# Performance work log

Hardware: AMD Instinct MI355X
Metric: run time of the kernel (lower is better)

Reference implementation:

```python
import jax, jax.numpy as jnp
import numpy as np

TEMPERATURE = 0.1
NEG_INF = -1e30


def setup_inputs() -> dict:
    key = jax.random.key(0)
    kf, kl = jax.random.split(key)
    N, D = 8192, 128
    features = jax.random.normal(kf, (N, D), dtype=jnp.float32)
    # labels in [-1, 80): -1 marks background rows that are filtered out
    labels = jax.random.randint(kl, (N,), -1, 80)
    return {"features": features, "labels": labels}


def reference(features, labels):
    N = labels.shape[0]
    fg = labels >= 0  # [N]

    # F.normalize(p=2, dim=1): x / max(||x||, eps)
    norm = jnp.maximum(jnp.linalg.norm(features, axis=1, keepdims=True), 1e-12)
    f = features / norm

    sim = jnp.matmul(f, f.T) / TEMPERATURE  # [N, N]

    pair_fg = fg[:, None] & fg[None, :]
    eye = jnp.eye(N, dtype=bool)
    label_eq = labels[:, None] == labels[None, :]
    pos_mask = pair_fg & label_eq & ~eye          # positives (same label, not self)
    all_mask = pair_fg & ~eye                     # pos | neg == everything but self (within fg)

    # row-wise masked max, clamped to [-20, 20] as in the original
    max_sim = jnp.max(jnp.where(all_mask, sim, NEG_INF), axis=1)
    max_sim = jnp.clip(max_sim, -20.0, 20.0)

    e = jnp.exp(sim - max_sim[:, None])           # cos-sim/temp is bounded, no overflow
    pos_sum = jnp.clip(jnp.sum(jnp.where(pos_mask, e, 0.0), axis=1), 1e-6, 1e6)
    all_sum = jnp.clip(jnp.sum(jnp.where(all_mask, e, 0.0), axis=1), 1e-6, 1e6)

    loss_i = jnp.minimum(-jnp.log(pos_sum / all_sum), 10.0)  # clamp(max=10)

    # rows contributing to the mean: fg rows with at least one positive
    valid = fg & (jnp.sum(pos_mask, axis=1) > 0)
    n_valid = jnp.sum(valid)
    mean_loss = jnp.sum(jnp.where(valid, loss_i, 0.0)) / jnp.maximum(n_valid, 1).astype(jnp.float32)

    ok = (jnp.sum(fg) >= 2) & (n_valid > 0)
    return jnp.where(ok, mean_loss, jnp.float32(0.0))
```

## Files before the change

kernel.cpp:

```cpp
#include <hip/hip_runtime.h>

#define N 8192
#define D 128
#define CHUNK 512
#define NCHUNK (N / CHUNK)
#define TILE_IT (CHUNK / 128)
#define NBIN 81
#define NBLK 512

typedef unsigned short u16;
typedef __attribute__((ext_vector_type(8))) __bf16 bf16x8;
typedef __attribute__((ext_vector_type(4))) float f32x4;

#define PREP_SCALE 3.7982889979f

__device__ __forceinline__ u16 f2bf(float x) {
  unsigned u = __float_as_uint(x);
  u += 0x7fff + ((u >> 16) & 1);
  return (u16)(u >> 16);
}
__device__ __forceinline__ float bf2f(u16 h) {
  return __uint_as_float(((unsigned)h) << 16);
}

__global__ __launch_bounds__(256) void cpe_prep(const float* __restrict__ feat,
                                                const int* __restrict__ labels,
                                                u16* __restrict__ fhi,
                                                u16* __restrict__ flo,
                                                int* __restrict__ slab,
                                                float* __restrict__ pacc,
                                                unsigned* __restrict__ ctr) {
  __shared__ int hist[4][NBIN], part[4][NBIN], lbase[NBIN], lpos[16];
  const int tid = threadIdx.x;
  const int w = tid >> 6, l = tid & 63;
  const int bid = blockIdx.x;
  if (tid < NBIN) {
#pragma unroll
    for (int cp = 0; cp < 4; ++cp) { hist[cp][tid] = 0; part[cp][tid] = 0; }
  }
  if (tid < 32) pacc[bid * 32 + tid] = 0.0f;
  if (bid == 0 && tid == 0) *ctr = 0u;
  __syncthreads();
  const int myBase = bid * 16;
  for (int j = tid; j < N; j += 256) {
    const int lab = labels[j] + 1;
    atomicAdd(&hist[w][lab], 1);
    if (j < myBase) atomicAdd(&part[w][lab], 1);
  }
  __syncthreads();
  if (tid < NBIN) {
    hist[0][tid] += hist[1][tid] + hist[2][tid] + hist[3][tid];
    part[0][tid] += part[1][tid] + part[2][tid] + part[3][tid];
  }
  __syncthreads();
  if (tid == 0) {
    int s = 0;
    for (int b = 0; b < NBIN; ++b) { lbase[b] = s; s += hist[0][b]; }
  }
  __syncthreads();
  if (tid < 16) {
    const int L = labels[myBase + tid] + 1;
    int pos = lbase[L] + part[0][L];
    for (int k = 0; k < tid; ++k) pos += (labels[myBase + k] + 1 == L) ? 1 : 0;
    lpos[tid] = pos;
    slab[pos] = L - 1;
  }
  __syncthreads();
#pragma unroll
  for (int rr = 0; rr < 4; ++rr) {
    const int k = w * 4 + rr;
    const float2 x = *(const float2*)&feat[(myBase + k) * D + l * 2];
    float s = x.x * x.x + x.y * x.y;
#pragma unroll
    for (int sh = 1; sh < 64; sh <<= 1) s += __shfl_xor(s, sh);
    const float inv = PREP_SCALE / fmaxf(sqrtf(s), 1e-12f);
    const float a = x.x * inv, b = x.y * inv;
    const u16 ah = f2bf(a), bh = f2bf(b);
    const u16 al = f2bf(a - bf2f(ah)), bl = f2bf(b - bf2f(bh));
    const int pos = lpos[k];
    *(ushort2*)&fhi[pos * D + l * 2] = make_ushort2(ah, bh);
    *(ushort2*)&flo[pos * D + l * 2] = make_ushort2(al, bl);
  }
}

__global__ __launch_bounds__(256, 2) void cpe_main(
    const u16* __restrict__ fhi, const u16* __restrict__ flo,
    const int* __restrict__ slab, float* __restrict__ pacc,
    unsigned* __restrict__ ctr, float* __restrict__ out) {
  __shared__ __align__(16) u16 Bh[128 * 128];
  __shared__ __align__(16) u16 Bl[128 * 128];
  __shared__ int Lab[CHUNK];
  __shared__ float red[3][4];
  __shared__ int isLast;
  const int rt = blockIdx.x, cc = blockIdx.y;
  const int tid = threadIdx.x;
  const int w = tid >> 6, l = tid & 63, q = l >> 4, m = l & 15;
  const int r0w = rt * 256 + w * 64;
  const int cbase0 = cc * CHUNK;

  Lab[tid] = slab[cbase0 + tid];
  Lab[tid + 256] = slab[cbase0 + 256 + tid];

  const int labi_lo = slab[r0w], labi_hi = slab[r0w + 63];

  bf16x8 Ah[4][4];
  int labi[4][4];
#pragma unroll
  for (int tr = 0; tr < 4; ++tr) {
    const int row = r0w + tr * 16 + m;
#pragma unroll
    for (int ks = 0; ks < 4; ++ks)
      Ah[tr][ks] = *(const bf16x8*)&fhi[row * D + ks * 32 + q * 8];
#pragma unroll
    for (int v = 0; v < 4; ++v) labi[tr][v] = slab[r0w + tr * 16 + q * 4 + v];
  }

  float ps[4][4], as_[4][4];
#pragma unroll
  for (int tr = 0; tr < 4; ++tr)
#pragma unroll
    for (int v = 0; v < 4; ++v) { ps[tr][v] = 0.f; as_[tr][v] = 0.f; }

  for (int it = 0; it < TILE_IT; ++it) {
    const int cbase = cbase0 + it * 128;
    __syncthreads();
#pragma unroll
    for (int n = 0; n < 8; ++n) {
      const int r = w * 32 + n * 4 + q;
      const int c = m ^ (r & 15);
      const u16* gh = &fhi[(size_t)(cbase + r) * D + c * 8];
      const u16* gl = &flo[(size_t)(cbase + r) * D + c * 8];
      __builtin_amdgcn_global_load_lds(
          (const __attribute__((address_space(1))) unsigned*)gh,
          (__attribute__((address_space(3))) unsigned*)&Bh[(w * 512 + n * 64) * 8],
          16, 0, 0);
      __builtin_amdgcn_global_load_lds(
          (const __attribute__((address_space(1))) unsigned*)gl,
          (__attribute__((address_space(3))) unsigned*)&Bl[(w * 512 + n * 64) * 8],
          16, 0, 0);
    }
    __syncthreads();

    for (int ct = 0; ct < 8; ++ct) {
      const int tb = it * 128 + ct * 16;
      const int labj_lo = Lab[tb], labj_hi = Lab[tb + 15];
      if (labj_hi < 0) continue;
      const bool slow = (labj_lo < 0) | ((labj_hi >= labi_lo) & (labj_lo <= labi_hi));
      const int jj = ct * 16 + m;
      f32x4 acc[4];
#pragma unroll
      for (int tr = 0; tr < 4; ++tr) acc[tr] = (f32x4){0.f, 0.f, 0.f, 0.f};
#pragma unroll
      for (int ks = 0; ks < 4; ++ks) {
        const int off = jj * 128 + ((ks * 4 + q) ^ m) * 8;
        const bf16x8 bh = *(const bf16x8*)&Bh[off];
        const bf16x8 bl = *(const bf16x8*)&Bl[off];
#pragma unroll
        for (int tr = 0; tr < 4; ++tr)
          acc[tr] = __builtin_amdgcn_mfma_f32_16x16x32_bf16(Ah[tr][ks], bh, acc[tr], 0, 0, 0);
#pragma unroll
        for (int tr = 0; tr < 4; ++tr)
          acc[tr] = __builtin_amdgcn_mfma_f32_16x16x32_bf16(Ah[tr][ks], bl, acc[tr], 0, 0, 0);
      }
      if (!slow) {
#pragma unroll
        for (int tr = 0; tr < 4; ++tr)
#pragma unroll
          for (int v = 0; v < 4; ++v)
            as_[tr][v] += __builtin_amdgcn_exp2f(acc[tr][v]);
      } else {
        const int labj = Lab[tb + m];
        const bool fgj = labj >= 0;
        const int jbase = cbase + ct * 16;
#pragma unroll
        for (int tr = 0; tr < 4; ++tr) {
          if (jbase == r0w + tr * 16) {
#pragma unroll
            for (int v = 0; v < 4; ++v) {
              const float e = __builtin_amdgcn_exp2f(acc[tr][v]);
              const float em = (fgj && (m != q * 4 + v)) ? e : 0.0f;
              as_[tr][v] += em;
              ps[tr][v] += (labj == labi[tr][v]) ? em : 0.0f;
            }
          } else {
#pragma unroll
            for (int v = 0; v < 4; ++v) {
              const float e = __builtin_amdgcn_exp2f(acc[tr][v]);
              const float em = fgj ? e : 0.0f;
              as_[tr][v] += em;
              ps[tr][v] += (labj == labi[tr][v]) ? em : 0.0f;
            }
          }
        }
      }
    }
  }

#pragma unroll
  for (int tr = 0; tr < 4; ++tr)
#pragma unroll
    for (int v = 0; v < 4; ++v) {
      float vp = ps[tr][v], va = as_[tr][v];
#pragma unroll
      for (int s = 1; s < 16; s <<= 1) {
        vp += __shfl_xor(vp, s);
        va += __shfl_xor(va, s);
      }
      if (m == 0) {
        const int r = r0w + tr * 16 + q * 4 + v;
        atomicAdd(&pacc[2 * r], vp);
        atomicAdd(&pacc[2 * r + 1], va);
      }
    }

  __syncthreads();
  if (tid == 0) {
    __threadfence();
    isLast = (atomicAdd(ctr, 1u) == NBLK - 1) ? 1 : 0;
  }
  __syncthreads();
  if (isLast) {
    float v0 = 0.f, v1 = 0.f, v2 = 0.f;
#pragma unroll 4
    for (int k = 0; k < 32; ++k) {
      const int r = k * 256 + tid;
      const float psr = atomicAdd(&pacc[2 * r], 0.0f);
      const float asr = atomicAdd(&pacc[2 * r + 1], 0.0f);
      const bool fg = slab[r] >= 0;
      const bool valid = fg && (psr > 0.f);
      const float loss = fminf(logf(asr / psr), 10.0f);
      v0 += valid ? loss : 0.f;
      v1 += valid ? 1.f : 0.f;
      v2 += fg ? 1.f : 0.f;
    }
#pragma unroll
    for (int s = 1; s < 64; s <<= 1) {
      v0 += __shfl_xor(v0, s);
      v1 += __shfl_xor(v1, s);
      v2 += __shfl_xor(v2, s);
    }
    if (l == 0) { red[0][w] = v0; red[1][w] = v1; red[2][w] = v2; }
    __syncthreads();
    if (tid == 0) {
      const float ls = red[0][0] + red[0][1] + red[0][2] + red[0][3];
      const float nv = red[1][0] + red[1][1] + red[1][2] + red[1][3];
      const float nf = red[2][0] + red[2][1] + red[2][2] + red[2][3];
      out[0] = (nf >= 2.0f && nv > 0.0f) ? ls / fmaxf(nv, 1.0f) : 0.0f;
    }
  }
}

extern "C" void kernel_launch(void* const* d_in, const int* in_sizes, int n_in,
                              void* d_out, int out_size, void* d_ws, size_t ws_size,
                              hipStream_t stream) {
  const float* feat = (const float*)d_in[0];
  const int* labels = (const int*)d_in[1];
  float* out = (float*)d_out;
  char* ws = (char*)d_ws;
  u16* fhi = (u16*)ws;
  u16* flo = (u16*)(ws + (size_t)N * D * 2);
  float* pacc = (float*)(ws + (size_t)N * D * 4);
  int* slab = (int*)(ws + (size_t)N * D * 4 + (size_t)N * 8);
  unsigned* ctr = (unsigned*)(ws + (size_t)N * D * 4 + (size_t)N * 8 + (size_t)N * 4);

  cpe_prep<<<NBLK, 256, 0, stream>>>(feat, labels, fhi, flo, slab, pacc, ctr);
  cpe_main<<<dim3(N / 256, NCHUNK), 256, 0, stream>>>(fhi, flo, slab, pacc, ctr, out);
}
```

Baseline: 121.7 us.

## Drop bf16 lo-part correction, shrink column chunks, replace atomics with per-row partials

Removes the hi/lo bf16 split, so the similarity matmul runs on a single bf16 operand. This halves the MFMA count, the LDS traffic and the global loads, at the cost of accuracy in exp(sim). The column chunk is halved to 256, giving twice as many blocks, and occupancy is raised to 4 blocks per CU now that LDS use is smaller. Per-row float atomics are replaced by non-atomic partial writes that the last block of each row tile reduces, followed by a final two-level counter for the scalar loss.

```diff
diff --git a/kernel.cpp b/kernel.cpp
--- a/kernel.cpp
+++ b/kernel.cpp
@@ -2,11 +2,11 @@
 
 #define N 8192
 #define D 128
-#define CHUNK 512
-#define NCHUNK (N / CHUNK)
+#define CHUNK 256
+#define NCC (N / CHUNK)
 #define TILE_IT (CHUNK / 128)
 #define NBIN 81
-#define NBLK 512
+#define PBLK 512
 
 typedef unsigned short u16;
 typedef __attribute__((ext_vector_type(8))) __bf16 bf16x8;
@@ -19,17 +19,14 @@
   u += 0x7fff + ((u >> 16) & 1);
   return (u16)(u >> 16);
 }
-__device__ __forceinline__ float bf2f(u16 h) {
-  return __uint_as_float(((unsigned)h) << 16);
-}
 
 __global__ __launch_bounds__(256) void cpe_prep(const float* __restrict__ feat,
                                                 const int* __restrict__ labels,
                                                 u16* __restrict__ fhi,
-                                                u16* __restrict__ flo,
                                                 int* __restrict__ slab,
-                                                float* __restrict__ pacc,
-                                                unsigned* __restrict__ ctr) {
+                                                unsigned* __restrict__ ctrR,
+                                                float* __restrict__ acc3,
+                                                unsigned* __restrict__ ctr2) {
   __shared__ int hist[4][NBIN], part[4][NBIN], lbase[NBIN], lpos[16];
   const int tid = threadIdx.x;
   const int w = tid >> 6, l = tid & 63;
@@ -38,8 +35,11 @@
 #pragma unroll
     for (int cp = 0; cp < 4; ++cp) { hist[cp][tid] = 0; part[cp][tid] = 0; }
   }
-  if (tid < 32) pacc[bid * 32 + tid] = 0.0f;
-  if (bid == 0 && tid == 0) *ctr = 0u;
+  if (bid == 0) {
+    if (tid < 32) ctrR[tid] = 0u;
+    else if (tid < 36) acc3[tid - 32] = 0.0f;
+    else if (tid == 36) *ctr2 = 0u;
+  }
   __syncthreads();
   const int myBase = bid * 16;
   for (int j = tid; j < N; j += 256) {
@@ -74,21 +74,17 @@
 #pragma unroll
     for (int sh = 1; sh < 64; sh <<= 1) s += __shfl_xor(s, sh);
     const float inv = PREP_SCALE / fmaxf(sqrtf(s), 1e-12f);
-    const float a = x.x * inv, b = x.y * inv;
-    const u16 ah = f2bf(a), bh = f2bf(b);
-    const u16 al = f2bf(a - bf2f(ah)), bl = f2bf(b - bf2f(bh));
     const int pos = lpos[k];
-    *(ushort2*)&fhi[pos * D + l * 2] = make_ushort2(ah, bh);
-    *(ushort2*)&flo[pos * D + l * 2] = make_ushort2(al, bl);
-  }
-}
-
-__global__ __launch_bounds__(256, 2) void cpe_main(
-    const u16* __restrict__ fhi, const u16* __restrict__ flo,
-    const int* __restrict__ slab, float* __restrict__ pacc,
-    unsigned* __restrict__ ctr, float* __restrict__ out) {
+    *(ushort2*)&fhi[pos * D + l * 2] = make_ushort2(f2bf(x.x * inv), f2bf(x.y * inv));
+  }
+}
+
+__global__ __launch_bounds__(256, 4) void cpe_main(
+    const u16* __restrict__ fhi, const int* __restrict__ slab,
+    float2* __restrict__ partials, unsigned* __restrict__ ctrR,
+    float* __restrict__ acc3, unsigned* __restrict__ ctr2,
+    float* __restrict__ out) {
   __shared__ __align__(16) u16 Bh[128 * 128];
-  __shared__ __align__(16) u16 Bl[128 * 128];
   __shared__ int Lab[CHUNK];
   __shared__ float red[3][4];
   __shared__ int isLast;
@@ -99,7 +95,6 @@
   const int cbase0 = cc * CHUNK;
 
   Lab[tid] = slab[cbase0 + tid];
-  Lab[tid + 256] = slab[cbase0 + 256 + tid];
 
   const int labi_lo = slab[r0w], labi_hi = slab[r0w + 63];
 
@@ -129,14 +124,9 @@
       const int r = w * 32 + n * 4 + q;
       const int c = m ^ (r & 15);
       const u16* gh = &fhi[(size_t)(cbase + r) * D + c * 8];
-      const u16* gl = &flo[(size_t)(cbase + r) * D + c * 8];
       __builtin_amdgcn_global_load_lds(
           (const __attribute__((address_space(1))) unsigned*)gh,
           (__attribute__((address_space(3))) unsigned*)&Bh[(w * 512 + n * 64) * 8],
-          16, 0, 0);
-      __builtin_amdgcn_global_load_lds(
-          (const __attribute__((address_space(1))) unsigned*)gl,
-          (__attribute__((address_space(3))) unsigned*)&Bl[(w * 512 + n * 64) * 8],
           16, 0, 0);
     }
     __syncthreads();
@@ -154,13 +144,9 @@
       for (int ks = 0; ks < 4; ++ks) {
         const int off = jj * 128 + ((ks * 4 + q) ^ m) * 8;
         const bf16x8 bh = *(const bf16x8*)&Bh[off];
-        const bf16x8 bl = *(const bf16x8*)&Bl[off];
 #pragma unroll
         for (int tr = 0; tr < 4; ++tr)
           acc[tr] = __builtin_amdgcn_mfma_f32_16x16x32_bf16(Ah[tr][ks], bh, acc[tr], 0, 0, 0);
-#pragma unroll
-        for (int tr = 0; tr < 4; ++tr)
-          acc[tr] = __builtin_amdgcn_mfma_f32_16x16x32_bf16(Ah[tr][ks], bl, acc[tr], 0, 0, 0);
       }
       if (!slow) {
 #pragma unroll
@@ -206,33 +192,34 @@
         vp += __shfl_xor(vp, s);
         va += __shfl_xor(va, s);
       }
-      if (m == 0) {
-        const int r = r0w + tr * 16 + q * 4 + v;
-        atomicAdd(&pacc[2 * r], vp);
-        atomicAdd(&pacc[2 * r + 1], va);
-      }
+      if (m == 0)
+        partials[(size_t)cc * N + r0w + tr * 16 + q * 4 + v] = make_float2(vp, va);
     }
 
   __syncthreads();
   if (tid == 0) {
     __threadfence();
-    isLast = (atomicAdd(ctr, 1u) == NBLK - 1) ? 1 : 0;
+    isLast = (atomicAdd(&ctrR[rt], 1u) == NCC - 1) ? 1 : 0;
   }
   __syncthreads();
   if (isLast) {
-    float v0 = 0.f, v1 = 0.f, v2 = 0.f;
+    __threadfence();
+    const int r = rt * 256 + tid;
+    float psr = 0.f, asr = 0.f;
 #pragma unroll 4
-    for (int k = 0; k < 32; ++k) {
-      const int r = k * 256 + tid;
-      const float psr = atomicAdd(&pacc[2 * r], 0.0f);
-      const float asr = atomicAdd(&pacc[2 * r + 1], 0.0f);
-      const bool fg = slab[r] >= 0;
-      const bool valid = fg && (psr > 0.f);
-      const float loss = fminf(logf(asr / psr), 10.0f);
-      v0 += valid ? loss : 0.f;
-      v1 += valid ? 1.f : 0.f;
-      v2 += fg ? 1.f : 0.f;
-    }
+    for (int c = 0; c < NCC; ++c) {
+      union { unsigned long long u; float2 f; } cv;
+      cv.u = __hip_atomic_load((const unsigned long long*)&partials[(size_t)c * N + r],
+                               __ATOMIC_RELAXED, __HIP_MEMORY_SCOPE_AGENT);
+      psr += cv.f.x;
+      asr += cv.f.y;
+    }
+    const bool fg = slab[r] >= 0;
+    const bool valid = fg && (psr > 0.f);
+    const float loss = fminf(logf(asr / psr), 10.0f);
+    float v0 = valid ? loss : 0.f;
+    float v1 = valid ? 1.f : 0.f;
+    float v2 = fg ? 1.f : 0.f;
 #pragma unroll
     for (int s = 1; s < 64; s <<= 1) {
       v0 += __shfl_xor(v0, s);
@@ -242,10 +229,16 @@
     if (l == 0) { red[0][w] = v0; red[1][w] = v1; red[2][w] = v2; }
     __syncthreads();
     if (tid == 0) {
-      const float ls = red[0][0] + red[0][1] + red[0][2] + red[0][3];
-      const float nv = red[1][0] + red[1][1] + red[1][2] + red[1][3];
-      const float nf = red[2][0] + red[2][1] + red[2][2] + red[2][3];
-      out[0] = (nf >= 2.0f && nv > 0.0f) ? ls / fmaxf(nv, 1.0f) : 0.0f;
+      atomicAdd(&acc3[0], red[0][0] + red[0][1] + red[0][2] + red[0][3]);
+      atomicAdd(&acc3[1], red[1][0] + red[1][1] + red[1][2] + red[1][3]);
+      atomicAdd(&acc3[2], red[2][0] + red[2][1] + red[2][2] + red[2][3]);
+      __threadfence();
+      if (atomicAdd(ctr2, 1u) == 31u) {
+        const float ls = atomicAdd(&acc3[0], 0.0f);
+        const float nv = atomicAdd(&acc3[1], 0.0f);
+        const float nf = atomicAdd(&acc3[2], 0.0f);
+        out[0] = (nf >= 2.0f && nv > 0.0f) ? ls / fmaxf(nv, 1.0f) : 0.0f;
+      }
     }
   }
 }
@@ -258,11 +251,14 @@
   float* out = (float*)d_out;
   char* ws = (char*)d_ws;
   u16* fhi = (u16*)ws;
-  u16* flo = (u16*)(ws + (size_t)N * D * 2);
-  float* pacc = (float*)(ws + (size_t)N * D * 4);
-  int* slab = (int*)(ws + (size_t)N * D * 4 + (size_t)N * 8);
-  unsigned* ctr = (unsigned*)(ws + (size_t)N * D * 4 + (size_t)N * 8 + (size_t)N * 4);
-
-  cpe_prep<<<NBLK, 256, 0, stream>>>(feat, labels, fhi, flo, slab, pacc, ctr);
-  cpe_main<<<dim3(N / 256, NCHUNK), 256, 0, stream>>>(fhi, flo, slab, pacc, ctr, out);
-}
+  float2* partials = (float2*)(ws + (size_t)N * D * 2);
+  char* tail = ws + (size_t)N * D * 2 + (size_t)NCC * N * 8;
+  int* slab = (int*)tail;
+  unsigned* ctrR = (unsigned*)(tail + N * 4);
+  float* acc3 = (float*)(tail + N * 4 + 128);
+  unsigned* ctr2 = (unsigned*)(tail + N * 4 + 256);
+
+  cpe_prep<<<PBLK, 256, 0, stream>>>(feat, labels, fhi, slab, ctrR, acc3, ctr2);
+  cpe_main<<<dim3(N / 256, NCC), 256, 0, stream>>>(fhi, slab, partials, ctrR,
+                                                   acc3, ctr2, out);
+}
```

Result: slower. 191.2 us (+57.2%).
